# Optimization experiments

Measured on AMD Instinct MI355X. Metric: run time of the kernel, lower is better.

The kernel has to match this reference:

```python
import jax, jax.numpy as jnp
import numpy as np

LN_EPS = 1e-5
BN_EPS = 1e-5


def setup_inputs() -> dict:
    key = jax.random.key(0)
    ks = jax.random.split(key, 16)
    N, C, T, H, W = 4, 256, 5, 28, 28
    Ci = 128
    CA = 128  # audio feature dim (hard-coded 128 in nn.Linear(128, in_channels))
    s = 0.02
    inp = {
        "x": jax.random.normal(ks[0], (N, C, T, H, W), jnp.float32),
        "audio": jax.random.normal(ks[1], (N, T, CA), jnp.float32),
        "align_W": jax.random.normal(ks[2], (C, CA), jnp.float32) * s,
        "align_b": jax.random.normal(ks[3], (C,), jnp.float32) * s,
        "g_W": jax.random.normal(ks[4], (Ci, C), jnp.float32) * s,
        "g_b": jax.random.normal(ks[5], (Ci,), jnp.float32) * s,
        "theta_W": jax.random.normal(ks[6], (Ci, C), jnp.float32) * s,
        "theta_b": jax.random.normal(ks[7], (Ci,), jnp.float32) * s,
        "phi_W": jax.random.normal(ks[8], (Ci, C), jnp.float32) * s,
        "phi_b": jax.random.normal(ks[9], (Ci,), jnp.float32) * s,
        "Wz_W": jax.random.normal(ks[10], (C, Ci), jnp.float32) * s,
        "Wz_b": jax.random.normal(ks[11], (C,), jnp.float32) * s,
        "bn_gamma": jax.random.normal(ks[12], (C,), jnp.float32) * s + 1.0,
        "bn_beta": jax.random.normal(ks[13], (C,), jnp.float32) * s,
        "bn_mean": jnp.zeros((C,), jnp.float32),
        "bn_var": jnp.ones((C,), jnp.float32),
        "ln_gamma": jnp.ones((C,), jnp.float32),
        "ln_beta": jnp.zeros((C,), jnp.float32),
    }
    return inp


def _tpavi(x, audio, align_W, align_b, g_W, g_b, theta_W, theta_b,
           phi_W, phi_b, Wz_W, Wz_b, bn_gamma, bn_beta, bn_mean, bn_var,
           ln_gamma, ln_beta):
    N, C, T, H, W = x.shape
    L = T * H * W
    # audio alignment: Linear(128 -> C), then broadcast over H, W
    audio_temp = jnp.einsum('ntc,oc->nto', audio, align_W) + align_b     # (N,T,C)
    a = audio_temp.transpose(0, 2, 1)[:, :, :, None, None]               # (N,C,T,1,1)
    a = jnp.broadcast_to(a, (N, C, T, H, W)).reshape(N, C, L)            # (N,C,L)

    xf = x.reshape(N, C, L)                                              # (N,C,L)
    # 1x1 conv3d == per-token channel mixing
    g_x = jnp.einsum('oc,ncl->nlo', g_W, xf) + g_b                       # (N,L,Ci)
    theta_x = jnp.einsum('oc,ncl->nlo', theta_W, xf) + theta_b           # (N,L,Ci)
    phi_x = jnp.einsum('oc,ncl->nol', phi_W, a) + phi_b[None, :, None]   # (N,Ci,L)

    # dot mode: f = theta phi^T, normalized by token count (no softmax)
    f = jnp.einsum('nlo,nok->nlk', theta_x, phi_x)                       # (N,L,L)
    f_div_C = f / L
    y = jnp.einsum('nlk,nko->nlo', f_div_C, g_x)                         # (N,L,Ci)

    y = y.transpose(0, 2, 1)                                             # (N,Ci,L)
    # W_z: 1x1 conv (Ci -> C) + BatchNorm3d (inference statistics)
    wy = jnp.einsum('oc,ncl->nol', Wz_W, y) + Wz_b[None, :, None]        # (N,C,L)
    inv = bn_gamma / jnp.sqrt(bn_var + BN_EPS)
    wy = (wy - bn_mean[None, :, None]) * inv[None, :, None] + bn_beta[None, :, None]

    z = wy.reshape(N, C, T, H, W) + x                                    # residual
    # LayerNorm over channel dim (channels-last in the original)
    zt = z.transpose(0, 2, 3, 4, 1)                                      # (N,T,H,W,C)
    mu = jnp.mean(zt, axis=-1, keepdims=True)
    var = jnp.mean(jnp.square(zt - mu), axis=-1, keepdims=True)
    zt = (zt - mu) / jnp.sqrt(var + LN_EPS) * ln_gamma + ln_beta
    z = zt.transpose(0, 4, 1, 2, 3)                                      # (N,C,T,H,W)
    return z, audio_temp


def reference(x, audio, align_W, align_b, g_W, g_b, theta_W, theta_b,
              phi_W, phi_b, Wz_W, Wz_b, bn_gamma, bn_beta, bn_mean, bn_var,
              ln_gamma, ln_beta):
    return _tpavi(x, audio, align_W, align_b, g_W, g_b, theta_W, theta_b,
                  phi_W, phi_b, Wz_W, Wz_b, bn_gamma, bn_beta, bn_mean, bn_var,
                  ln_gamma, ln_beta)
```

## Files before the change

### kernel.cpp

```cpp
#include <hip/hip_runtime.h>

#define N_DIM 4
#define C_DIM 256
#define T_DIM 5
#define HW    784
#define L_TOK 3920
#define CI    128
#define CA    128

#define WS_XS  0
#define WS_TP  5120
#define WS_GW  10240
#define WS_TB  15360

__global__ __launch_bounds__(256) void k1_xsum(const float* __restrict__ x,
                                               float* __restrict__ ws) {
    int bid = blockIdx.x;
    int n   = bid / (C_DIM * T_DIM);
    int rem = bid % (C_DIM * T_DIM);
    int c   = rem / T_DIM;
    int t   = rem % T_DIM;
    const float4* base = (const float4*)(x + ((size_t)(n * C_DIM + c) * T_DIM + t) * HW);
    int tid = threadIdx.x;

    float p = 0.f;
    if (tid < HW / 4) {
        float4 v = base[tid];
        p = (v.x + v.y) + (v.z + v.w);
    }
    for (int off = 32; off > 0; off >>= 1) p += __shfl_down(p, off, 64);
    __shared__ float wsum[4];
    if ((tid & 63) == 0) wsum[tid >> 6] = p;
    __syncthreads();
    if (tid == 0) {
        ws[WS_XS + (n * T_DIM + t) * C_DIM + c] = wsum[0] + wsum[1] + wsum[2] + wsum[3];
    }
}

__global__ __launch_bounds__(256) void k2_small(
    const float* __restrict__ audio,   const float* __restrict__ align_W,
    const float* __restrict__ align_b, const float* __restrict__ g_W,
    const float* __restrict__ g_b,     const float* __restrict__ theta_W,
    const float* __restrict__ theta_b, const float* __restrict__ phi_W,
    const float* __restrict__ phi_b,   const float* __restrict__ Wz_W,
    const float* __restrict__ bn_gamma,const float* __restrict__ bn_var,
    float* __restrict__ ws, float* __restrict__ out_audio) {
    int nt = blockIdx.x;
    int tid = threadIdx.x;

    __shared__ float audio_s[CA];
    __shared__ float at_s[C_DIM];
    __shared__ float xs_s[C_DIM];
    __shared__ float phi_s[CI];
    __shared__ float g_s[CI];

    if (tid < CA) audio_s[tid] = audio[nt * CA + tid];
    xs_s[tid] = ws[WS_XS + nt * C_DIM + tid];
    __syncthreads();

    {
        const float4* row = (const float4*)(align_W + tid * CA);
        float a0 = 0, a1 = 0, a2 = 0, a3 = 0;
        #pragma unroll
        for (int k = 0; k < CA / 4; ++k) {
            float4 w = row[k];
            a0 = fmaf(w.x, audio_s[4 * k + 0], a0);
            a1 = fmaf(w.y, audio_s[4 * k + 1], a1);
            a2 = fmaf(w.z, audio_s[4 * k + 2], a2);
            a3 = fmaf(w.w, audio_s[4 * k + 3], a3);
        }
        float acc = align_b[tid] + (a0 + a1) + (a2 + a3);
        at_s[tid] = acc;
        out_audio[nt * C_DIM + tid] = acc;
    }
    __syncthreads();

    if (tid < CI) {
        const float4* prow = (const float4*)(phi_W + tid * C_DIM);
        const float4* grow = (const float4*)(g_W + tid * C_DIM);
        float p0 = 0, p1 = 0, p2 = 0, p3 = 0;
        float q0 = 0, q1 = 0, q2 = 0, q3 = 0;
        #pragma unroll
        for (int k = 0; k < C_DIM / 4; ++k) {
            float4 w = prow[k];
            float4 u = grow[k];
            float b0 = at_s[4 * k + 0], b1 = at_s[4 * k + 1];
            float b2 = at_s[4 * k + 2], b3 = at_s[4 * k + 3];
            float c0 = xs_s[4 * k + 0], c1 = xs_s[4 * k + 1];
            float c2 = xs_s[4 * k + 2], c3 = xs_s[4 * k + 3];
            p0 = fmaf(w.x, b0, p0); p1 = fmaf(w.y, b1, p1);
            p2 = fmaf(w.z, b2, p2); p3 = fmaf(w.w, b3, p3);
            q0 = fmaf(u.x, c0, q0); q1 = fmaf(u.y, c1, q1);
            q2 = fmaf(u.z, c2, q2); q3 = fmaf(u.w, c3, q3);
        }
        phi_s[tid] = phi_b[tid] + (p0 + p1) + (p2 + p3);
        g_s[tid]   = (float)HW * g_b[tid] + (q0 + q1) + (q2 + q3);
    }
    __syncthreads();

    {
        float a0 = 0, a1 = 0, a2 = 0, a3 = 0;
        #pragma unroll 4
        for (int o = 0; o < CI; o += 4) {
            a0 = fmaf(theta_W[(o + 0) * C_DIM + tid], phi_s[o + 0], a0);
            a1 = fmaf(theta_W[(o + 1) * C_DIM + tid], phi_s[o + 1], a1);
            a2 = fmaf(theta_W[(o + 2) * C_DIM + tid], phi_s[o + 2], a2);
            a3 = fmaf(theta_W[(o + 3) * C_DIM + tid], phi_s[o + 3], a3);
        }
        ws[WS_TP + nt * C_DIM + tid] = (a0 + a1) + (a2 + a3);
    }
    if (tid < 64) {
        float p = theta_b[tid] * phi_s[tid] + theta_b[tid + 64] * phi_s[tid + 64];
        for (int off = 32; off > 0; off >>= 1) p += __shfl_down(p, off, 64);
        if (tid == 0) ws[WS_TB + nt] = p;
    }
    {
        const float4* row = (const float4*)(Wz_W + tid * CI);
        float a0 = 0, a1 = 0, a2 = 0, a3 = 0;
        #pragma unroll
        for (int k = 0; k < CI / 4; ++k) {
            float4 w = row[k];
            a0 = fmaf(w.x, g_s[4 * k + 0], a0);
            a1 = fmaf(w.y, g_s[4 * k + 1], a1);
            a2 = fmaf(w.z, g_s[4 * k + 2], a2);
            a3 = fmaf(w.w, g_s[4 * k + 3], a3);
        }
        float inv = bn_gamma[tid] * rsqrtf(bn_var[tid] + 1e-5f);
        ws[WS_GW + nt * C_DIM + tid] = ((a0 + a1) + (a2 + a3)) * inv * (1.0f / (float)L_TOK);
    }
}

__global__ __launch_bounds__(1024) void k3_main(
    const float* __restrict__ x,        const float* __restrict__ ws,
    const float* __restrict__ Wz_b,     const float* __restrict__ bn_gamma,
    const float* __restrict__ bn_beta,  const float* __restrict__ bn_mean,
    const float* __restrict__ bn_var,   const float* __restrict__ ln_gamma,
    const float* __restrict__ ln_beta,  float* __restrict__ out) {
    __shared__ float TPs[T_DIM * C_DIM];
    __shared__ float GWs[T_DIM * C_DIM];
    __shared__ float tb_s[T_DIM];
    __shared__ float B_s[C_DIM], lng_s[C_DIM], lnb_s[C_DIM];
    __shared__ float Fp[T_DIM * 1024];
    __shared__ float Sp[2 * 1024];

    int n    = blockIdx.y;
    int tile = blockIdx.x;
    int tid  = threadIdx.x;
    int g    = tid >> 6;
    int li   = tid & 63;
    int l    = tile * 64 + li;
    bool act = (l < L_TOK);

    for (int i = tid; i < T_DIM * C_DIM; i += 1024) {
        TPs[i] = ws[WS_TP + n * T_DIM * C_DIM + i];
        GWs[i] = ws[WS_GW + n * T_DIM * C_DIM + i];
    }
    if (tid < T_DIM) tb_s[tid] = ws[WS_TB + n * T_DIM + tid];
    if (tid < C_DIM) {
        int c = tid;
        float inv = bn_gamma[c] * rsqrtf(bn_var[c] + 1e-5f);
        B_s[c]   = (Wz_b[c] - bn_mean[c]) * inv + bn_beta[c];
        lng_s[c] = ln_gamma[c];
        lnb_s[c] = ln_beta[c];
    }
    __syncthreads();

    float xz[16];
    const float* xb = x + ((size_t)(n * C_DIM + g * 16)) * L_TOK + l;
    #pragma unroll
    for (int j = 0; j < 16; ++j) xz[j] = act ? xb[(size_t)j * L_TOK] : 0.f;

    float F0 = 0, F1 = 0, F2 = 0, F3 = 0, F4 = 0;
    #pragma unroll
    for (int j = 0; j < 16; ++j) {
        const float* tp = TPs + g * 16 + j;
        F0 = fmaf(xz[j], tp[0],    F0);
        F1 = fmaf(xz[j], tp[256],  F1);
        F2 = fmaf(xz[j], tp[512],  F2);
        F3 = fmaf(xz[j], tp[768],  F3);
        F4 = fmaf(xz[j], tp[1024], F4);
    }
    Fp[0 * 1024 + tid] = F0; Fp[1 * 1024 + tid] = F1; Fp[2 * 1024 + tid] = F2;
    Fp[3 * 1024 + tid] = F3; Fp[4 * 1024 + tid] = F4;
    __syncthreads();

    float Ft[T_DIM];
    #pragma unroll
    for (int t = 0; t < T_DIM; ++t) {
        float a = tb_s[t];
        #pragma unroll
        for (int w = 0; w < 16; ++w) a += Fp[t * 1024 + w * 64 + li];
        Ft[t] = a;
    }
    float s1 = 0.f, s2 = 0.f;
    #pragma unroll
    for (int j = 0; j < 16; ++j) {
        int c = g * 16 + j;
        float zc = B_s[c] + xz[j];
        zc = fmaf(Ft[0], GWs[c],        zc);
        zc = fmaf(Ft[1], GWs[256 + c],  zc);
        zc = fmaf(Ft[2], GWs[512 + c],  zc);
        zc = fmaf(Ft[3], GWs[768 + c],  zc);
        zc = fmaf(Ft[4], GWs[1024 + c], zc);
        xz[j] = zc;
        s1 += zc;
        s2 = fmaf(zc, zc, s2);
    }
    Sp[tid]        = s1;
    Sp[1024 + tid] = s2;
    __syncthreads();

    float t1 = 0.f, t2 = 0.f;
    #pragma unroll
    for (int w = 0; w < 16; ++w) {
        t1 += Sp[w * 64 + li];
        t2 += Sp[1024 + w * 64 + li];
    }
    float mu   = t1 * (1.0f / C_DIM);
    float var  = t2 * (1.0f / C_DIM) - mu * mu;
    float rstd = rsqrtf(var + 1e-5f);
    if (act) {
        float* ob = out + ((size_t)(n * C_DIM + g * 16)) * L_TOK + l;
        #pragma unroll
        for (int j = 0; j < 16; ++j) {
            int c = g * 16 + j;
            ob[(size_t)j * L_TOK] = fmaf((xz[j] - mu) * rstd, lng_s[c], lnb_s[c]);
        }
    }
}

extern "C" void kernel_launch(void* const* d_in, const int* in_sizes, int n_in,
                              void* d_out, int out_size, void* d_ws, size_t ws_size,
                              hipStream_t stream) {
    const float* x        = (const float*)d_in[0];
    const float* audio    = (const float*)d_in[1];
    const float* align_W  = (const float*)d_in[2];
    const float* align_b  = (const float*)d_in[3];
    const float* g_W      = (const float*)d_in[4];
    const float* g_b      = (const float*)d_in[5];
    const float* theta_W  = (const float*)d_in[6];
    const float* theta_b  = (const float*)d_in[7];
    const float* phi_W    = (const float*)d_in[8];
    const float* phi_b    = (const float*)d_in[9];
    const float* Wz_W     = (const float*)d_in[10];
    const float* Wz_b     = (const float*)d_in[11];
    const float* bn_gamma = (const float*)d_in[12];
    const float* bn_beta  = (const float*)d_in[13];
    const float* bn_mean  = (const float*)d_in[14];
    const float* bn_var   = (const float*)d_in[15];
    const float* ln_gamma = (const float*)d_in[16];
    const float* ln_beta  = (const float*)d_in[17];

    float* out       = (float*)d_out;
    float* out_audio = out + (size_t)N_DIM * C_DIM * L_TOK;
    float* ws        = (float*)d_ws;

    k1_xsum<<<N_DIM * C_DIM * T_DIM, 256, 0, stream>>>(x, ws);
    k2_small<<<N_DIM * T_DIM, 256, 0, stream>>>(
        audio, align_W, align_b, g_W, g_b, theta_W, theta_b, phi_W, phi_b,
        Wz_W, bn_gamma, bn_var, ws, out_audio);
    dim3 grid3((L_TOK + 63) / 64, N_DIM);
    k3_main<<<grid3, 1024, 0, stream>>>(
        x, ws, Wz_b, bn_gamma, bn_beta, bn_mean, bn_var, ln_gamma, ln_beta, out);
}
```

Before: 136.0 us.

## Fuse small projection kernel into main kernel with pre-transposed weights

Removes the separate low-parallelism kernel that computed audio alignment, phi/g projections and theta/Wz folds, and instead has every main-kernel block recompute them redundantly from weights transposed into workspace by the first kernel. This eliminates one launch and the serial dependency on a 20-block kernel. In exchange each block does extra matvec work, reads about half a megabyte of weights from cache, and uses more shared memory, which may lower occupancy.

```diff
diff --git a/kernel.cpp b/kernel.cpp
--- a/kernel.cpp
+++ b/kernel.cpp
@@ -8,138 +8,70 @@
 #define CI    128
 #define CA    128
 
-#define WS_XS  0
-#define WS_TP  5120
-#define WS_GW  10240
-#define WS_TB  15360
-
-__global__ __launch_bounds__(256) void k1_xsum(const float* __restrict__ x,
-                                               float* __restrict__ ws) {
+#define WS_XS   0
+#define WS_TR   8192
+
+__global__ __launch_bounds__(256) void kA(const float* __restrict__ x,
+                                          const float* __restrict__ align_W,
+                                          const float* __restrict__ phi_W,
+                                          const float* __restrict__ g_W,
+                                          const float* __restrict__ Wz_W,
+                                          float* __restrict__ ws) {
     int bid = blockIdx.x;
-    int n   = bid / (C_DIM * T_DIM);
-    int rem = bid % (C_DIM * T_DIM);
-    int c   = rem / T_DIM;
-    int t   = rem % T_DIM;
-    const float4* base = (const float4*)(x + ((size_t)(n * C_DIM + c) * T_DIM + t) * HW);
     int tid = threadIdx.x;
-
-    float p = 0.f;
-    if (tid < HW / 4) {
-        float4 v = base[tid];
-        p = (v.x + v.y) + (v.z + v.w);
-    }
-    for (int off = 32; off > 0; off >>= 1) p += __shfl_down(p, off, 64);
-    __shared__ float wsum[4];
-    if ((tid & 63) == 0) wsum[tid >> 6] = p;
-    __syncthreads();
-    if (tid == 0) {
-        ws[WS_XS + (n * T_DIM + t) * C_DIM + c] = wsum[0] + wsum[1] + wsum[2] + wsum[3];
+    if (bid < N_DIM * C_DIM * T_DIM) {
+        int n   = bid / (C_DIM * T_DIM);
+        int rem = bid % (C_DIM * T_DIM);
+        int c   = rem / T_DIM;
+        int t   = rem % T_DIM;
+        const float4* base = (const float4*)(x + ((size_t)(n * C_DIM + c) * T_DIM + t) * HW);
+        float p = 0.f;
+        if (tid < HW / 4) {
+            float4 v = base[tid];
+            p = (v.x + v.y) + (v.z + v.w);
+        }
+        for (int off = 32; off > 0; off >>= 1) p += __shfl_down(p, off, 64);
+        __shared__ float wsum[4];
+        if ((tid & 63) == 0) wsum[tid >> 6] = p;
+        __syncthreads();
+        if (tid == 0)
+            ws[WS_XS + (n * T_DIM + t) * C_DIM + c] = wsum[0] + wsum[1] + wsum[2] + wsum[3];
+    } else {
+        int tb = bid - N_DIM * C_DIM * T_DIM;
+        #pragma unroll
+        for (int k = 0; k < 4; ++k) {
+            int D = tb * 1024 + k * 256 + tid;
+            int m = D >> 15;
+            int r = D & 32767;
+            float v;
+            if (m == 0)      { int a = r >> 8, c = r & 255; v = align_W[c * CA + a]; }
+            else if (m == 1) { int c = r >> 7, o = r & 127; v = phi_W[o * C_DIM + c]; }
+            else if (m == 2) { int c = r >> 7, o = r & 127; v = g_W[o * C_DIM + c]; }
+            else             { int o = r >> 8, c = r & 255; v = Wz_W[c * CI + o]; }
+            ws[WS_TR + D] = v;
+        }
     }
 }
 
-__global__ __launch_bounds__(256) void k2_small(
-    const float* __restrict__ audio,   const float* __restrict__ align_W,
-    const float* __restrict__ align_b, const float* __restrict__ g_W,
-    const float* __restrict__ g_b,     const float* __restrict__ theta_W,
-    const float* __restrict__ theta_b, const float* __restrict__ phi_W,
-    const float* __restrict__ phi_b,   const float* __restrict__ Wz_W,
-    const float* __restrict__ bn_gamma,const float* __restrict__ bn_var,
-    float* __restrict__ ws, float* __restrict__ out_audio) {
-    int nt = blockIdx.x;
-    int tid = threadIdx.x;
-
-    __shared__ float audio_s[CA];
-    __shared__ float at_s[C_DIM];
-    __shared__ float xs_s[C_DIM];
-    __shared__ float phi_s[CI];
-    __shared__ float g_s[CI];
-
-    if (tid < CA) audio_s[tid] = audio[nt * CA + tid];
-    xs_s[tid] = ws[WS_XS + nt * C_DIM + tid];
-    __syncthreads();
-
-    {
-        const float4* row = (const float4*)(align_W + tid * CA);
-        float a0 = 0, a1 = 0, a2 = 0, a3 = 0;
-        #pragma unroll
-        for (int k = 0; k < CA / 4; ++k) {
-            float4 w = row[k];
-            a0 = fmaf(w.x, audio_s[4 * k + 0], a0);
-            a1 = fmaf(w.y, audio_s[4 * k + 1], a1);
-            a2 = fmaf(w.z, audio_s[4 * k + 2], a2);
-            a3 = fmaf(w.w, audio_s[4 * k + 3], a3);
-        }
-        float acc = align_b[tid] + (a0 + a1) + (a2 + a3);
-        at_s[tid] = acc;
-        out_audio[nt * C_DIM + tid] = acc;
-    }
-    __syncthreads();
-
-    if (tid < CI) {
-        const float4* prow = (const float4*)(phi_W + tid * C_DIM);
-        const float4* grow = (const float4*)(g_W + tid * C_DIM);
-        float p0 = 0, p1 = 0, p2 = 0, p3 = 0;
-        float q0 = 0, q1 = 0, q2 = 0, q3 = 0;
-        #pragma unroll
-        for (int k = 0; k < C_DIM / 4; ++k) {
-            float4 w = prow[k];
-            float4 u = grow[k];
-            float b0 = at_s[4 * k + 0], b1 = at_s[4 * k + 1];
-            float b2 = at_s[4 * k + 2], b3 = at_s[4 * k + 3];
-            float c0 = xs_s[4 * k + 0], c1 = xs_s[4 * k + 1];
-            float c2 = xs_s[4 * k + 2], c3 = xs_s[4 * k + 3];
-            p0 = fmaf(w.x, b0, p0); p1 = fmaf(w.y, b1, p1);
-            p2 = fmaf(w.z, b2, p2); p3 = fmaf(w.w, b3, p3);
-            q0 = fmaf(u.x, c0, q0); q1 = fmaf(u.y, c1, q1);
-            q2 = fmaf(u.z, c2, q2); q3 = fmaf(u.w, c3, q3);
-        }
-        phi_s[tid] = phi_b[tid] + (p0 + p1) + (p2 + p3);
-        g_s[tid]   = (float)HW * g_b[tid] + (q0 + q1) + (q2 + q3);
-    }
-    __syncthreads();
-
-    {
-        float a0 = 0, a1 = 0, a2 = 0, a3 = 0;
-        #pragma unroll 4
-        for (int o = 0; o < CI; o += 4) {
-            a0 = fmaf(theta_W[(o + 0) * C_DIM + tid], phi_s[o + 0], a0);
-            a1 = fmaf(theta_W[(o + 1) * C_DIM + tid], phi_s[o + 1], a1);
-            a2 = fmaf(theta_W[(o + 2) * C_DIM + tid], phi_s[o + 2], a2);
-            a3 = fmaf(theta_W[(o + 3) * C_DIM + tid], phi_s[o + 3], a3);
-        }
-        ws[WS_TP + nt * C_DIM + tid] = (a0 + a1) + (a2 + a3);
-    }
-    if (tid < 64) {
-        float p = theta_b[tid] * phi_s[tid] + theta_b[tid + 64] * phi_s[tid + 64];
-        for (int off = 32; off > 0; off >>= 1) p += __shfl_down(p, off, 64);
-        if (tid == 0) ws[WS_TB + nt] = p;
-    }
-    {
-        const float4* row = (const float4*)(Wz_W + tid * CI);
-        float a0 = 0, a1 = 0, a2 = 0, a3 = 0;
-        #pragma unroll
-        for (int k = 0; k < CI / 4; ++k) {
-            float4 w = row[k];
-            a0 = fmaf(w.x, g_s[4 * k + 0], a0);
-            a1 = fmaf(w.y, g_s[4 * k + 1], a1);
-            a2 = fmaf(w.z, g_s[4 * k + 2], a2);
-            a3 = fmaf(w.w, g_s[4 * k + 3], a3);
-        }
-        float inv = bn_gamma[tid] * rsqrtf(bn_var[tid] + 1e-5f);
-        ws[WS_GW + nt * C_DIM + tid] = ((a0 + a1) + (a2 + a3)) * inv * (1.0f / (float)L_TOK);
-    }
-}
-
-__global__ __launch_bounds__(1024) void k3_main(
+__global__ __launch_bounds__(1024) void kB(
     const float* __restrict__ x,        const float* __restrict__ ws,
+    const float* __restrict__ audio,    const float* __restrict__ align_b,
+    const float* __restrict__ g_b,      const float* __restrict__ theta_W,
+    const float* __restrict__ theta_b,  const float* __restrict__ phi_b,
     const float* __restrict__ Wz_b,     const float* __restrict__ bn_gamma,
     const float* __restrict__ bn_beta,  const float* __restrict__ bn_mean,
     const float* __restrict__ bn_var,   const float* __restrict__ ln_gamma,
-    const float* __restrict__ ln_beta,  float* __restrict__ out) {
+    const float* __restrict__ ln_beta,  float* __restrict__ out,
+    float* __restrict__ out_audio) {
+    __shared__ float audio_s[T_DIM * CA];
+    __shared__ float xs_s[T_DIM * C_DIM];
+    __shared__ float at_s[T_DIM * C_DIM];
+    __shared__ float phi_s[T_DIM * CI];
+    __shared__ float g2_s[T_DIM * CI];
     __shared__ float TPs[T_DIM * C_DIM];
     __shared__ float GWs[T_DIM * C_DIM];
     __shared__ float tb_s[T_DIM];
-    __shared__ float B_s[C_DIM], lng_s[C_DIM], lnb_s[C_DIM];
+    __shared__ float B_s[C_DIM], inv_s[C_DIM], lng_s[C_DIM], lnb_s[C_DIM];
     __shared__ float Fp[T_DIM * 1024];
     __shared__ float Sp[2 * 1024];
 
@@ -151,17 +83,78 @@
     int l    = tile * 64 + li;
     bool act = (l < L_TOK);
 
-    for (int i = tid; i < T_DIM * C_DIM; i += 1024) {
-        TPs[i] = ws[WS_TP + n * T_DIM * C_DIM + i];
-        GWs[i] = ws[WS_GW + n * T_DIM * C_DIM + i];
-    }
-    if (tid < T_DIM) tb_s[tid] = ws[WS_TB + n * T_DIM + tid];
+    const float* alignT = ws + WS_TR;
+    const float* phiT   = ws + WS_TR + 32768;
+    const float* gT     = ws + WS_TR + 65536;
+    const float* WzT    = ws + WS_TR + 98304;
+
+    if (tid < T_DIM * CA) audio_s[tid] = audio[n * T_DIM * CA + tid];
+    for (int i = tid; i < T_DIM * C_DIM; i += 1024) xs_s[i] = ws[WS_XS + n * T_DIM * C_DIM + i];
     if (tid < C_DIM) {
         int c = tid;
         float inv = bn_gamma[c] * rsqrtf(bn_var[c] + 1e-5f);
+        inv_s[c] = inv * (1.0f / (float)L_TOK);
         B_s[c]   = (Wz_b[c] - bn_mean[c]) * inv + bn_beta[c];
         lng_s[c] = ln_gamma[c];
         lnb_s[c] = ln_beta[c];
+    }
+    __syncthreads();
+
+    for (int i = tid; i < T_DIM * C_DIM; i += 1024) {
+        int t = i >> 8, c = i & 255;
+        float a0 = 0, a1 = 0, a2 = 0, a3 = 0;
+        const float* as = audio_s + t * CA;
+        #pragma unroll 8
+        for (int a = 0; a < CA; a += 4) {
+            a0 = fmaf(alignT[(a + 0) * C_DIM + c], as[a + 0], a0);
+            a1 = fmaf(alignT[(a + 1) * C_DIM + c], as[a + 1], a1);
+            a2 = fmaf(alignT[(a + 2) * C_DIM + c], as[a + 2], a2);
+            a3 = fmaf(alignT[(a + 3) * C_DIM + c], as[a + 3], a3);
+        }
+        float v = align_b[c] + (a0 + a1) + (a2 + a3);
+        at_s[i] = v;
+        if (tile == 0) out_audio[n * T_DIM * C_DIM + i] = v;
+    }
+    __syncthreads();
+
+    if (tid < T_DIM * CI) {
+        int t = tid >> 7, o = tid & 127;
+        const float* ats = at_s + t * C_DIM;
+        const float* xss = xs_s + t * C_DIM;
+        float p0 = 0, p1 = 0, q0 = 0, q1 = 0;
+        #pragma unroll 8
+        for (int c = 0; c < C_DIM; c += 2) {
+            p0 = fmaf(phiT[(c + 0) * CI + o], ats[c + 0], p0);
+            p1 = fmaf(phiT[(c + 1) * CI + o], ats[c + 1], p1);
+            q0 = fmaf(gT[(c + 0) * CI + o],  xss[c + 0], q0);
+            q1 = fmaf(gT[(c + 1) * CI + o],  xss[c + 1], q1);
+        }
+        phi_s[tid] = phi_b[o] + p0 + p1;
+        g2_s[tid]  = (float)HW * g_b[o] + q0 + q1;
+    }
+    __syncthreads();
+
+    for (int i = tid; i < T_DIM * C_DIM; i += 1024) {
+        int t = i >> 8, c = i & 255;
+        const float* ps = phi_s + t * CI;
+        const float* gs = g2_s + t * CI;
+        float a0 = 0, a1 = 0, b0 = 0, b1 = 0;
+        #pragma unroll 8
+        for (int o = 0; o < CI; o += 2) {
+            a0 = fmaf(theta_W[(o + 0) * C_DIM + c], ps[o + 0], a0);
+            a1 = fmaf(theta_W[(o + 1) * C_DIM + c], ps[o + 1], a1);
+            b0 = fmaf(WzT[(o + 0) * C_DIM + c],     gs[o + 0], b0);
+            b1 = fmaf(WzT[(o + 1) * C_DIM + c],     gs[o + 1], b1);
+        }
+        TPs[i] = a0 + a1;
+        GWs[i] = (b0 + b1) * inv_s[c];
+    }
+    if (tid < T_DIM * 64) {
+        int t = tid >> 6, lane = tid & 63;
+        float p = theta_b[lane] * phi_s[t * CI + lane] +
+                  theta_b[lane + 64] * phi_s[t * CI + lane + 64];
+        for (int off = 32; off > 0; off >>= 1) p += __shfl_down(p, off, 64);
+        if (lane == 0) tb_s[t] = p;
     }
     __syncthreads();
 
@@ -255,11 +248,10 @@
     float* out_audio = out + (size_t)N_DIM * C_DIM * L_TOK;
     float* ws        = (float*)d_ws;
 
-    k1_xsum<<<N_DIM * C_DIM * T_DIM, 256, 0, stream>>>(x, ws);
-    k2_small<<<N_DIM * T_DIM, 256, 0, stream>>>(
-        audio, align_W, align_b, g_W, g_b, theta_W, theta_b, phi_W, phi_b,
-        Wz_W, bn_gamma, bn_var, ws, out_audio);
-    dim3 grid3((L_TOK + 63) / 64, N_DIM);
-    k3_main<<<grid3, 1024, 0, stream>>>(
-        x, ws, Wz_b, bn_gamma, bn_beta, bn_mean, bn_var, ln_gamma, ln_beta, out);
+    kA<<<N_DIM * C_DIM * T_DIM + 128, 256, 0, stream>>>(x, align_W, phi_W, g_W, Wz_W, ws);
+    dim3 gridB((L_TOK + 63) / 64, N_DIM);
+    kB<<<gridB, 1024, 0, stream>>>(
+        x, ws, audio, align_b, g_b, theta_W, theta_b, phi_b,
+        Wz_b, bn_gamma, bn_beta, bn_mean, bn_var, ln_gamma, ln_beta,
+        out, out_audio);
 }
```

Result: no change. 137.5 us (+1.2%).

## Move audio projection into xsum kernel and widen small-matvec kernel to 1024 threads

Applied to the files above, without the earlier changes.

The audio alignment linear layer moves out of the serial small kernel and runs as 20 extra blocks of the x-sum kernel, writing its result to workspace. The small kernel now uses 1024 threads per block. It splits each phi/g and theta/Wz mat-vec across 4 or 2 lanes with shuffle reductions, which shortens the serial dependency chain in this latency-bound stage. This costs an extra workspace round trip and loses float4 weight loads, with uncoalesced access for some rows.

```diff
diff --git a/kernel.cpp b/kernel.cpp
--- a/kernel.cpp
+++ b/kernel.cpp
@@ -9,56 +9,41 @@
 #define CA    128
 
 #define WS_XS  0
-#define WS_TP  5120
-#define WS_GW  10240
-#define WS_TB  15360
-
-__global__ __launch_bounds__(256) void k1_xsum(const float* __restrict__ x,
-                                               float* __restrict__ ws) {
+#define WS_AT  5120
+#define WS_TP  10240
+#define WS_GW  15360
+#define WS_TB  20480
+
+__global__ __launch_bounds__(256) void k1(const float* __restrict__ x,
+                                          const float* __restrict__ audio,
+                                          const float* __restrict__ align_W,
+                                          const float* __restrict__ align_b,
+                                          float* __restrict__ ws,
+                                          float* __restrict__ out_audio) {
     int bid = blockIdx.x;
-    int n   = bid / (C_DIM * T_DIM);
-    int rem = bid % (C_DIM * T_DIM);
-    int c   = rem / T_DIM;
-    int t   = rem % T_DIM;
-    const float4* base = (const float4*)(x + ((size_t)(n * C_DIM + c) * T_DIM + t) * HW);
     int tid = threadIdx.x;
-
-    float p = 0.f;
-    if (tid < HW / 4) {
-        float4 v = base[tid];
-        p = (v.x + v.y) + (v.z + v.w);
-    }
-    for (int off = 32; off > 0; off >>= 1) p += __shfl_down(p, off, 64);
-    __shared__ float wsum[4];
-    if ((tid & 63) == 0) wsum[tid >> 6] = p;
-    __syncthreads();
-    if (tid == 0) {
-        ws[WS_XS + (n * T_DIM + t) * C_DIM + c] = wsum[0] + wsum[1] + wsum[2] + wsum[3];
-    }
-}
-
-__global__ __launch_bounds__(256) void k2_small(
-    const float* __restrict__ audio,   const float* __restrict__ align_W,
-    const float* __restrict__ align_b, const float* __restrict__ g_W,
-    const float* __restrict__ g_b,     const float* __restrict__ theta_W,
-    const float* __restrict__ theta_b, const float* __restrict__ phi_W,
-    const float* __restrict__ phi_b,   const float* __restrict__ Wz_W,
-    const float* __restrict__ bn_gamma,const float* __restrict__ bn_var,
-    float* __restrict__ ws, float* __restrict__ out_audio) {
-    int nt = blockIdx.x;
-    int tid = threadIdx.x;
-
-    __shared__ float audio_s[CA];
-    __shared__ float at_s[C_DIM];
-    __shared__ float xs_s[C_DIM];
-    __shared__ float phi_s[CI];
-    __shared__ float g_s[CI];
-
-    if (tid < CA) audio_s[tid] = audio[nt * CA + tid];
-    xs_s[tid] = ws[WS_XS + nt * C_DIM + tid];
-    __syncthreads();
-
-    {
+    if (bid < N_DIM * C_DIM * T_DIM) {
+        int n   = bid / (C_DIM * T_DIM);
+        int rem = bid % (C_DIM * T_DIM);
+        int c   = rem / T_DIM;
+        int t   = rem % T_DIM;
+        const float4* base = (const float4*)(x + ((size_t)(n * C_DIM + c) * T_DIM + t) * HW);
+        float p = 0.f;
+        if (tid < HW / 4) {
+            float4 v = base[tid];
+            p = (v.x + v.y) + (v.z + v.w);
+        }
+        for (int off = 32; off > 0; off >>= 1) p += __shfl_down(p, off, 64);
+        __shared__ float wsum[4];
+        if ((tid & 63) == 0) wsum[tid >> 6] = p;
+        __syncthreads();
+        if (tid == 0)
+            ws[WS_XS + (n * T_DIM + t) * C_DIM + c] = wsum[0] + wsum[1] + wsum[2] + wsum[3];
+    } else {
+        int nt = bid - N_DIM * C_DIM * T_DIM;
+        __shared__ float audio_s[CA];
+        if (tid < CA) audio_s[tid] = audio[nt * CA + tid];
+        __syncthreads();
         const float4* row = (const float4*)(align_W + tid * CA);
         float a0 = 0, a1 = 0, a2 = 0, a3 = 0;
         #pragma unroll
@@ -70,63 +55,88 @@
             a3 = fmaf(w.w, audio_s[4 * k + 3], a3);
         }
         float acc = align_b[tid] + (a0 + a1) + (a2 + a3);
-        at_s[tid] = acc;
+        ws[WS_AT + nt * C_DIM + tid] = acc;
         out_audio[nt * C_DIM + tid] = acc;
     }
-    __syncthreads();
-
-    if (tid < CI) {
-        const float4* prow = (const float4*)(phi_W + tid * C_DIM);
-        const float4* grow = (const float4*)(g_W + tid * C_DIM);
-        float p0 = 0, p1 = 0, p2 = 0, p3 = 0;
-        float q0 = 0, q1 = 0, q2 = 0, q3 = 0;
-        #pragma unroll
-        for (int k = 0; k < C_DIM / 4; ++k) {
-            float4 w = prow[k];
-            float4 u = grow[k];
-            float b0 = at_s[4 * k + 0], b1 = at_s[4 * k + 1];
-            float b2 = at_s[4 * k + 2], b3 = at_s[4 * k + 3];
-            float c0 = xs_s[4 * k + 0], c1 = xs_s[4 * k + 1];
-            float c2 = xs_s[4 * k + 2], c3 = xs_s[4 * k + 3];
-            p0 = fmaf(w.x, b0, p0); p1 = fmaf(w.y, b1, p1);
-            p2 = fmaf(w.z, b2, p2); p3 = fmaf(w.w, b3, p3);
-            q0 = fmaf(u.x, c0, q0); q1 = fmaf(u.y, c1, q1);
-            q2 = fmaf(u.z, c2, q2); q3 = fmaf(u.w, c3, q3);
-        }
-        phi_s[tid] = phi_b[tid] + (p0 + p1) + (p2 + p3);
-        g_s[tid]   = (float)HW * g_b[tid] + (q0 + q1) + (q2 + q3);
-    }
+}
+
+__global__ __launch_bounds__(1024) void k2(
+    const float* __restrict__ g_W,     const float* __restrict__ g_b,
+    const float* __restrict__ theta_W, const float* __restrict__ theta_b,
+    const float* __restrict__ phi_W,   const float* __restrict__ phi_b,
+    const float* __restrict__ Wz_W,    const float* __restrict__ bn_gamma,
+    const float* __restrict__ bn_var,  float* __restrict__ ws) {
+    int nt  = blockIdx.x;
+    int tid = threadIdx.x;
+
+    __shared__ float at_s[C_DIM];
+    __shared__ float xs_s[C_DIM];
+    __shared__ float phi_s[CI];
+    __shared__ float g_s[CI];
+
+    if (tid < C_DIM) at_s[tid] = ws[WS_AT + nt * C_DIM + tid];
+    else if (tid < 2 * C_DIM) xs_s[tid - C_DIM] = ws[WS_XS + nt * C_DIM + (tid - C_DIM)];
     __syncthreads();
 
     {
-        float a0 = 0, a1 = 0, a2 = 0, a3 = 0;
-        #pragma unroll 4
-        for (int o = 0; o < CI; o += 4) {
-            a0 = fmaf(theta_W[(o + 0) * C_DIM + tid], phi_s[o + 0], a0);
-            a1 = fmaf(theta_W[(o + 1) * C_DIM + tid], phi_s[o + 1], a1);
-            a2 = fmaf(theta_W[(o + 2) * C_DIM + tid], phi_s[o + 2], a2);
-            a3 = fmaf(theta_W[(o + 3) * C_DIM + tid], phi_s[o + 3], a3);
-        }
-        ws[WS_TP + nt * C_DIM + tid] = (a0 + a1) + (a2 + a3);
-    }
+        int half = tid >> 9;
+        int o    = (tid >> 2) & 127;
+        int s    = tid & 3;
+        const float* wrow = (half == 0 ? phi_W : g_W) + o * C_DIM + s * 64;
+        const float* vec  = (half == 0 ? at_s : xs_s) + s * 64;
+        float v0 = 0, v1 = 0;
+        #pragma unroll
+        for (int i = 0; i < 64; i += 2) {
+            v0 = fmaf(wrow[i + 0], vec[i + 0], v0);
+            v1 = fmaf(wrow[i + 1], vec[i + 1], v1);
+        }
+        float v = v0 + v1;
+        v += __shfl_xor(v, 1, 64);
+        v += __shfl_xor(v, 2, 64);
+        if (s == 0) {
+            if (half == 0) phi_s[o] = phi_b[o] + v;
+            else           g_s[o]   = (float)HW * g_b[o] + v;
+        }
+    }
+    __syncthreads();
+
+    {
+        int half = tid >> 9;
+        int c    = (tid >> 1) & 255;
+        int s    = tid & 1;
+        float v0 = 0, v1 = 0;
+        if (half == 0) {
+            const float* ps = phi_s + s * 64;
+            #pragma unroll
+            for (int i = 0; i < 64; i += 2) {
+                v0 = fmaf(theta_W[(s * 64 + i + 0) * C_DIM + c], ps[i + 0], v0);
+                v1 = fmaf(theta_W[(s * 64 + i + 1) * C_DIM + c], ps[i + 1], v1);
+            }
+        } else {
+            const float* wr = Wz_W + c * CI + s * 64;
+            const float* gs = g_s + s * 64;
+            #pragma unroll
+            for (int i = 0; i < 64; i += 2) {
+                v0 = fmaf(wr[i + 0], gs[i + 0], v0);
+                v1 = fmaf(wr[i + 1], gs[i + 1], v1);
+            }
+        }
+        float v = v0 + v1;
+        v += __shfl_xor(v, 1, 64);
+        if (s == 0) {
+            if (half == 0) {
+                ws[WS_TP + nt * C_DIM + c] = v;
+            } else {
+                float inv = bn_gamma[c] * rsqrtf(bn_var[c] + 1e-5f);
+                ws[WS_GW + nt * C_DIM + c] = v * inv * (1.0f / (float)L_TOK);
+            }
+        }
+    }
+    __syncthreads();
     if (tid < 64) {
         float p = theta_b[tid] * phi_s[tid] + theta_b[tid + 64] * phi_s[tid + 64];
         for (int off = 32; off > 0; off >>= 1) p += __shfl_down(p, off, 64);
         if (tid == 0) ws[WS_TB + nt] = p;
-    }
-    {
-        const float4* row = (const float4*)(Wz_W + tid * CI);
-        float a0 = 0, a1 = 0, a2 = 0, a3 = 0;
-        #pragma unroll
-        for (int k = 0; k < CI / 4; ++k) {
-            float4 w = row[k];
-            a0 = fmaf(w.x, g_s[4 * k + 0], a0);
-            a1 = fmaf(w.y, g_s[4 * k + 1], a1);
-            a2 = fmaf(w.z, g_s[4 * k + 2], a2);
-            a3 = fmaf(w.w, g_s[4 * k + 3], a3);
-        }
-        float inv = bn_gamma[tid] * rsqrtf(bn_var[tid] + 1e-5f);
-        ws[WS_GW + nt * C_DIM + tid] = ((a0 + a1) + (a2 + a3)) * inv * (1.0f / (float)L_TOK);
     }
 }
 
@@ -255,10 +265,10 @@
     float* out_audio = out + (size_t)N_DIM * C_DIM * L_TOK;
     float* ws        = (float*)d_ws;
 
-    k1_xsum<<<N_DIM * C_DIM * T_DIM, 256, 0, stream>>>(x, ws);
-    k2_small<<<N_DIM * T_DIM, 256, 0, stream>>>(
-        audio, align_W, align_b, g_W, g_b, theta_W, theta_b, phi_W, phi_b,
-        Wz_W, bn_gamma, bn_var, ws, out_audio);
+    k1<<<N_DIM * C_DIM * T_DIM + N_DIM * T_DIM, 256, 0, stream>>>(
+        x, audio, align_W, align_b, ws, out_audio);
+    k2<<<N_DIM * T_DIM, 1024, 0, stream>>>(
+        g_W, g_b, theta_W, theta_b, phi_W, phi_b, Wz_W, bn_gamma, bn_var, ws);
     dim3 grid3((L_TOK + 63) / 64, N_DIM);
     k3_main<<<grid3, 1024, 0, stream>>>(
         x, ws, Wz_b, bn_gamma, bn_beta, bn_mean, bn_var, ln_gamma, ln_beta, out);
```

Measured after the change: 135.3 us. About the same (-0.5%).
